# Optimization experiments

Measured on AMD Instinct MI355X. Metric: run time of the kernel, lower is better.

## Reference

```python
import jax, jax.numpy as jnp
import numpy as np

L_ITERS = 8   # number of ReduNet layers
C = 10        # number of classes
D = 1024      # feature dimension
N = 4096      # number of samples (columns of Z)


def setup_inputs() -> dict:
    key = jax.random.key(0)
    k0, k1, k2, k3 = jax.random.split(key, 4)
    Z = jax.random.normal(k0, (D, N), dtype=jnp.float32)
    # column-normalized features, as the net maintains at every layer
    Z = Z / jnp.linalg.norm(Z, axis=0, keepdims=True)
    # Elist[l]: (D,D) expansion operator; Cslist[l]: (C,D,D) per-class compression operators
    Elist = jax.random.normal(k1, (L_ITERS, D, D), dtype=jnp.float32) / np.float32(np.sqrt(D))
    Cslist = jax.random.normal(k2, (L_ITERS, C, D, D), dtype=jnp.float32) / np.float32(np.sqrt(D))
    gamma = jax.random.uniform(k3, (C,), dtype=jnp.float32)
    gamma = gamma / jnp.sum(gamma)
    eta = jnp.asarray(0.5, dtype=jnp.float32)
    temperature = jnp.asarray(0.1, dtype=jnp.float32)
    return {"Z": Z, "Elist": Elist, "Cslist": Cslist, "gamma": gamma,
            "eta": eta, "temperature": temperature, "L": L_ITERS}


def reference(Z, Elist, Cslist, gamma, eta, temperature, L):
    for l in range(L):
        Cs = Cslist[l]                                   # (C, d, d)
        CZ = jnp.einsum('cij,jn->cin', Cs, Z)            # (C, d, n)
        sims = -jnp.sqrt(jnp.sum(CZ * CZ, axis=1))       # fro norm over dim=1 -> (C, n)
        P_hat = jax.nn.softmax(sims / temperature, axis=0)  # softmax over classes
        PZ = P_hat[:, None, :] * Z                       # (C, d, n)
        term = jnp.einsum('c,cij,cjn->in', gamma, Cs, PZ)   # gamma-weighted class compression
        grads = Elist[l] @ Z - term                      # (d, n)
        Z = Z + eta * grads
        Z = Z / jnp.linalg.norm(Z, axis=0, keepdims=True)   # column-wise normalization
    return Z
```

## Files before the change

kernel.cpp:

```cpp
#include <hip/hip_runtime.h>
#include <hip/hip_bf16.h>
#include <stdint.h>

#define D_DIM 1024
#define N_DIM 4096
#define C_CLS 10
#define L_IT 8
#define M_DIM 11264
#define NBM 44

typedef __bf16 bf16_t;
typedef __bf16 bf16x8 __attribute__((ext_vector_type(8)));
typedef __bf16 bf16x4 __attribute__((ext_vector_type(4)));
typedef float  f32x4  __attribute__((ext_vector_type(4)));
typedef unsigned short u16x8 __attribute__((ext_vector_type(8)));

__device__ __forceinline__ float bf2f(uint16_t u) {
  union { uint32_t i; float f; } x; x.i = ((uint32_t)u) << 16; return x.f;
}

__global__ __launch_bounds__(256) void pack_w(const float4* __restrict__ Cs,
                                              const float4* __restrict__ El,
                                              bf16x4* __restrict__ dst) {
  const int CS4 = C_CLS * D_DIM * D_DIM / 4;
  int i = blockIdx.x * 256 + threadIdx.x;
  float4 v = (i < CS4) ? Cs[i] : El[i - CS4];
  bf16x4 o;
  o[0] = (bf16_t)v.x; o[1] = (bf16_t)v.y; o[2] = (bf16_t)v.z; o[3] = (bf16_t)v.w;
  dst[i] = o;
}

__global__ __launch_bounds__(256) void init_zt(const float* __restrict__ Zin,
                                               float* __restrict__ ZfT,
                                               bf16_t* __restrict__ ZbT) {
  __shared__ float tile[32][33];
  int tx = threadIdx.x & 31, ty = threadIdx.x >> 5;
  int nb = blockIdx.x, db = blockIdx.y;
  int n = nb * 32 + tx;
#pragma unroll
  for (int j = 0; j < 32; j += 8) {
    int d = db * 32 + ty + j;
    tile[ty + j][tx] = Zin[(size_t)d * N_DIM + n];
  }
  __syncthreads();
  int d2 = db * 32 + tx;
#pragma unroll
  for (int j = 0; j < 32; j += 8) {
    int n2 = nb * 32 + ty + j;
    float v = tile[tx][ty + j];
    ZfT[(size_t)n2 * D_DIM + d2] = v;
    ZbT[(size_t)n2 * D_DIM + d2] = (bf16_t)v;
  }
}

__global__ __launch_bounds__(256) void final_out(const float* __restrict__ ZfT,
                                                 float* __restrict__ outp) {
  __shared__ float tile[32][33];
  int tx = threadIdx.x & 31, ty = threadIdx.x >> 5;
  int nb = blockIdx.x, db = blockIdx.y;
#pragma unroll
  for (int j = 0; j < 32; j += 8) {
    int n = nb * 32 + ty + j;
    int d = db * 32 + tx;
    tile[ty + j][tx] = ZfT[(size_t)n * D_DIM + d];
  }
  __syncthreads();
#pragma unroll
  for (int j = 0; j < 32; j += 8) {
    int d2 = db * 32 + ty + j;
    int n2 = nb * 32 + tx;
    outp[(size_t)d2 * N_DIM + n2] = tile[tx][ty + j];
  }
}


#define STAGE_A(buf, h, t) do {                                                         \
    _Pragma("unroll") for (int e_ = 0; e_ < 2; ++e_) {                                  \
      const bf16_t* s_ = Wb + aoff0[e_] + (size_t)(h) * 65536 + (size_t)(t) * 64;       \
      __builtin_amdgcn_global_load_lds(                                                 \
        (const __attribute__((address_space(1))) void*)s_,                              \
        (__attribute__((address_space(3))) void*)(lds + (buf)*16384 + (h)*8192 + dstslot[e_]), \
        16, 0, 0);                                                                      \
    } } while (0)

#define STAGE_B(buf, h, t) do {                                                         \
    _Pragma("unroll") for (int e_ = 0; e_ < 2; ++e_) {                                  \
      const bf16_t* s_ = ZbT + boff0[e_] + (size_t)(h) * 32768 + (size_t)(t) * 64;      \
      __builtin_amdgcn_global_load_lds(                                                 \
        (const __attribute__((address_space(1))) void*)s_,                              \
        (__attribute__((address_space(3))) void*)(lds + 32768 + (buf)*16384 + (h)*8192 + dstslot[e_]), \
        16, 0, 0);                                                                      \
    } } while (0)

#define LOAD_A(buf, qm) do {                                                            \
    _Pragma("unroll") for (int f_ = 0; f_ < 4; ++f_)                                    \
      _Pragma("unroll") for (int kk_ = 0; kk_ < 2; ++kk_)                               \
        a[f_][kk_] = *(const bf16x8*)(lds + (buf)*16384 + (qm)*8192 + aRowBase + f_*1024 + sidx[kk_]); \
  } while (0)

#define LOAD_Bq(buf, qn, arr) do {                                                      \
    _Pragma("unroll") for (int f_ = 0; f_ < 2; ++f_)                                    \
      _Pragma("unroll") for (int kk_ = 0; kk_ < 2; ++kk_)                               \
        arr[f_][kk_] = *(const bf16x8*)(lds + 32768 + (buf)*16384 + (qn)*8192 + bRowBase + f_*1024 + sidx[kk_]); \
  } while (0)

#define MFMA_Q(qm, qn, arr) do {                                                        \
    _Pragma("unroll") for (int mm_ = 0; mm_ < 4; ++mm_)                                 \
      _Pragma("unroll") for (int nn_ = 0; nn_ < 2; ++nn_)                               \
        _Pragma("unroll") for (int kk_ = 0; kk_ < 2; ++kk_)                             \
          acc[(qm)*4+mm_][(qn)*2+nn_] = __builtin_amdgcn_mfma_f32_16x16x32_bf16(        \
            a[mm_][kk_], arr[nn_][kk_], acc[(qm)*4+mm_][(qn)*2+nn_], 0, 0, 0);          \
  } while (0)

#define PHASE(qm, qn, arr, LOAD_STMT, STAGE_STMT, WAIT_STMT) do {                       \
    LOAD_STMT;                                                                          \
    STAGE_STMT;                                                                         \
    __builtin_amdgcn_s_barrier();                                                       \
    asm volatile("s_waitcnt lgkmcnt(0)" ::: "memory");                                  \
    __builtin_amdgcn_sched_barrier(0);                                                  \
    __builtin_amdgcn_s_setprio(1);                                                      \
    MFMA_Q(qm, qn, arr);                                                                \
    __builtin_amdgcn_s_setprio(0);                                                      \
    WAIT_STMT;                                                                          \
    __builtin_amdgcn_s_barrier();                                                       \
  } while (0)

__global__ __launch_bounds__(512, 2) void gemm_wz8(const bf16_t* __restrict__ Wb,
                                                   const bf16_t* __restrict__ ZbT,
                                                   bf16_t* __restrict__ OUT_T, int ldn,
                                                   float* __restrict__ ssq) {
  __shared__ __align__(16) bf16_t lds[65536];

  int nwg = gridDim.x;
  int bid = blockIdx.x;
  int q = nwg >> 3, r = nwg & 7;
  int xcd = bid & 7, idx = bid >> 3;
  int swz = (xcd < r ? xcd * (q + 1) : r * (q + 1) + (xcd - r) * q) + idx;
  int bm = swz % NBM, bn = swz / NBM;
  int m0 = bm * 256, n0 = bn * 256;

  int tid = threadIdx.x;
  int wave = tid >> 6, lane = tid & 63;
  int wrow = wave >> 2, wcol = wave & 3;
  int lm = lane & 15, lks = lane >> 4;
  int sw = lm & 7;

  size_t aoff0[2], boff0[2];
  int dstslot[2];
#pragma unroll
  for (int e = 0; e < 2; ++e) {
    int j = e * 512 + tid;
    int rih = j >> 3, sl = j & 7;
    int sg = sl ^ (rih & 7);
    int arow = (rih & 63) + ((rih >> 6) << 7);
    int brow = (rih & 31) + ((rih >> 5) << 6);
    aoff0[e] = (size_t)(m0 + arow) * 1024 + sg * 8;
    boff0[e] = (size_t)(n0 + brow) * 1024 + sg * 8;
    dstslot[e] = e * 4096 + wave * 512;
  }

  int aRowBase = (wrow * 64 + lm) * 64;
  int bRowBase = (wcol * 32 + lm) * 64;
  int sidx[2] = { ((0 + lks) ^ sw) * 8, ((4 + lks) ^ sw) * 8 };

  f32x4 acc[8][4] = {};
  bf16x8 a[4][2], b0[2][2], b1[2][2];

  STAGE_A(0, 0, 0); STAGE_A(0, 1, 0); STAGE_B(0, 0, 0); STAGE_B(0, 1, 0);
  STAGE_A(1, 0, 1); STAGE_B(1, 0, 1);
  asm volatile("s_waitcnt vmcnt(4)" ::: "memory");
  __builtin_amdgcn_s_barrier();

  for (int it = 0; it < 7; ++it) {
    int tO = 2 * it + 1, tN = 2 * it + 2, tM = 2 * it + 3;
    PHASE(0, 0, b0, LOAD_A(0,0); LOAD_Bq(0,0,b0), STAGE_A(1, 1, tO), );
    PHASE(0, 1, b1, LOAD_Bq(0,1,b1),              STAGE_B(1, 1, tO), );
    PHASE(1, 0, b0, LOAD_A(0,1),                  STAGE_A(0, 0, tN), );
    PHASE(1, 1, b1, ,                             STAGE_A(0, 1, tN), asm volatile("s_waitcnt vmcnt(4)" ::: "memory"));
    PHASE(0, 0, b0, LOAD_A(1,0); LOAD_Bq(1,0,b0), STAGE_B(0, 0, tN), );
    PHASE(0, 1, b1, LOAD_Bq(1,1,b1),              STAGE_B(0, 1, tN), );
    PHASE(1, 0, b0, LOAD_A(1,1),                  STAGE_A(1, 0, tM), );
    PHASE(1, 1, b1, ,                             STAGE_B(1, 0, tM), asm volatile("s_waitcnt vmcnt(4)" ::: "memory"));
  }
  PHASE(0, 0, b0, LOAD_A(0,0); LOAD_Bq(0,0,b0), STAGE_A(1, 1, 15), );
  PHASE(0, 1, b1, LOAD_Bq(0,1,b1),              STAGE_B(1, 1, 15), );
  PHASE(1, 0, b0, LOAD_A(0,1),                  , );
  PHASE(1, 1, b1, ,                             , asm volatile("s_waitcnt vmcnt(0)" ::: "memory"));
  PHASE(0, 0, b0, LOAD_A(1,0); LOAD_Bq(1,0,b0), , );
  PHASE(0, 1, b1, LOAD_Bq(1,1,b1),              , );
  PHASE(1, 0, b0, LOAD_A(1,1),                  , );
  PHASE(1, 1, b1, ,                             , );

#pragma unroll
  for (int mf = 0; mf < 8; ++mf)
#pragma unroll
    for (int nf = 0; nf < 4; ++nf) {
      int col = n0 + wcol * 64 + nf * 16 + lm;
      int row = m0 + wrow * 128 + mf * 16 + lks * 4;
      bf16x4 v;
#pragma unroll
      for (int rr = 0; rr < 4; ++rr) v[rr] = (bf16_t)acc[mf][nf][rr];
      *(bf16x4*)(OUT_T + (size_t)col * M_DIM + row) = v;
    }

  if (m0 < C_CLS * 1024) {
    int c = m0 >> 10;
#pragma unroll
    for (int nf = 0; nf < 4; ++nf) {
      float v = 0.f;
#pragma unroll
      for (int mf = 0; mf < 8; ++mf)
#pragma unroll
        for (int rr = 0; rr < 4; ++rr)
          v += acc[mf][nf][rr] * acc[mf][nf][rr];
      v += __shfl_xor(v, 16);
      v += __shfl_xor(v, 32);
      if (lks == 0)
        atomicAdd(&ssq[(size_t)c * ldn + n0 + wcol * 64 + nf * 16 + lm], v);
    }
  }
}

__global__ __launch_bounds__(256) void update2(const bf16_t* __restrict__ OUT_T, int Nc,
                                               const float* __restrict__ ssq,
                                               const float* __restrict__ gamma,
                                               const float* __restrict__ etap,
                                               const float* __restrict__ tempr,
                                               float* __restrict__ ZfT,
                                               bf16_t* __restrict__ ZbT,
                                               int n_off) {
  int wv = threadIdx.x >> 6, lane = threadIdx.x & 63;
  int nl = blockIdx.x * 4 + wv;
  if (nl >= Nc) return;
  int n = n_off + nl;
  float eta = etap[0], invT = 1.0f / tempr[0];

  float s[C_CLS], m = -1e30f;
#pragma unroll
  for (int c = 0; c < C_CLS; ++c) {
    float sim = -sqrtf(ssq[(size_t)c * Nc + nl]);
    s[c] = sim;
    m = fmaxf(m, sim);
  }
  float sum = 0.f;
#pragma unroll
  for (int c = 0; c < C_CLS; ++c) {
    float e = __expf((s[c] - m) * invT);
    s[c] = e;
    sum += e;
  }
  float invsum = 1.0f / sum;
  float gP[C_CLS];
#pragma unroll
  for (int c = 0; c < C_CLS; ++c) gP[c] = gamma[c] * s[c] * invsum;

  const u16x8* ob = (const u16x8*)(OUT_T + (size_t)nl * M_DIM) + lane * 2;
  float term[16] = {};
#pragma unroll
  for (int c = 0; c < C_CLS; ++c) {
    u16x8 v0 = ob[c * 128], v1 = ob[c * 128 + 1];
#pragma unroll
    for (int j = 0; j < 8; ++j) {
      term[j]     += gP[c] * bf2f(v0[j]);
      term[8 + j] += gP[c] * bf2f(v1[j]);
    }
  }
  u16x8 g0 = ob[C_CLS * 128], g1 = ob[C_CLS * 128 + 1];

  const f32x4* zp = (const f32x4*)(ZfT + (size_t)n * D_DIM) + lane * 4;
  f32x4 z[4] = { zp[0], zp[1], zp[2], zp[3] };

  float zn[16];
  float ss = 0.f;
#pragma unroll
  for (int j = 0; j < 16; ++j) {
    float g = bf2f(j < 8 ? g0[j & 7] : g1[j & 7]);
    float v = z[j >> 2][j & 3] + eta * (g - term[j]);
    zn[j] = v;
    ss += v * v;
  }
#pragma unroll
  for (int k = 1; k < 64; k <<= 1) ss += __shfl_xor(ss, k);
  float inv = rsqrtf(ss);

  f32x4* zo = (f32x4*)(ZfT + (size_t)n * D_DIM) + lane * 4;
  bf16x8* bo = (bf16x8*)(ZbT + (size_t)n * D_DIM) + lane * 2;
#pragma unroll
  for (int q4 = 0; q4 < 4; ++q4) {
    f32x4 o;
#pragma unroll
    for (int j = 0; j < 4; ++j) o[j] = zn[q4 * 4 + j] * inv;
    zo[q4] = o;
  }
#pragma unroll
  for (int h = 0; h < 2; ++h) {
    bf16x8 o;
#pragma unroll
    for (int j = 0; j < 8; ++j) o[j] = (bf16_t)(zn[h * 8 + j] * inv);
    bo[h] = o;
  }
}

extern "C" void kernel_launch(void* const* d_in, const int* in_sizes, int n_in,
                              void* d_out, int out_size, void* d_ws, size_t ws_size,
                              hipStream_t stream) {
  (void)in_sizes; (void)n_in; (void)out_size;
  const float* Zin        = (const float*)d_in[0];
  const float* Elist      = (const float*)d_in[1];
  const float* Cslist     = (const float*)d_in[2];
  const float* gamma      = (const float*)d_in[3];
  const float* eta        = (const float*)d_in[4];
  const float* temperature= (const float*)d_in[5];

  auto align256 = [](size_t x) { return (x + 255) & ~(size_t)255; };
  size_t zbt_b = align256((size_t)N_DIM * D_DIM * 2);
  size_t zft_b = align256((size_t)N_DIM * D_DIM * 4);
  size_t wb_b  = align256((size_t)M_DIM * D_DIM * 2);
  size_t ssq_b = align256((size_t)L_IT * C_CLS * N_DIM * 4);
  size_t out_b = align256((size_t)M_DIM * N_DIM * 2);

  if (zbt_b + zft_b + wb_b + ssq_b + out_b > ws_size) {
    hipMemsetAsync(d_out, 0, (size_t)D_DIM * N_DIM * 4, stream);
    return;
  }

  char* p = (char*)d_ws;
  bf16_t* ZbT  = (bf16_t*)p; p += zbt_b;
  float*  ZfT  = (float*)p;  p += zft_b;
  bf16_t* Wb   = (bf16_t*)p; p += wb_b;
  float*  ssq  = (float*)p;  p += ssq_b;
  bf16_t* OUT_T= (bf16_t*)p;

  hipMemsetAsync(ssq, 0, (size_t)L_IT * C_CLS * N_DIM * 4, stream);
  init_zt<<<dim3(N_DIM / 32, D_DIM / 32), 256, 0, stream>>>(Zin, ZfT, ZbT);

  for (int l = 0; l < L_IT; ++l) {
    const float* Cs = Cslist + (size_t)l * C_CLS * D_DIM * D_DIM;
    const float* El = Elist  + (size_t)l * D_DIM * D_DIM;
    float* ssq_l = ssq + (size_t)l * C_CLS * N_DIM;

    pack_w<<<dim3(M_DIM * D_DIM / 4 / 256), 256, 0, stream>>>(
        (const float4*)Cs, (const float4*)El, (bf16x4*)Wb);

    gemm_wz8<<<dim3(NBM * (N_DIM / 256)), 512, 0, stream>>>(
        Wb, ZbT, OUT_T, N_DIM, ssq_l);
    update2<<<dim3(N_DIM / 4), 256, 0, stream>>>(
        OUT_T, N_DIM, ssq_l, gamma, eta, temperature, ZfT, ZbT, 0);
  }
  final_out<<<dim3(N_DIM / 32, D_DIM / 32), 256, 0, stream>>>(ZfT, (float*)d_out);
}
```

Measured before the change: 1.244 ms.

## Make the GEMM persistent over 256 workgroups and prefetch the next tile across tiles

Replaces the 704-workgroup GEMM launch with a persistent kernel of 256 workgroups. Each workgroup processes 2-3 output tiles inside its XCD-grouped range and stages the next tile's first K-slices during the tail of the current one, so the pipeline prologue and epilogue are overlapped. The phase schedule is also reworked to issue both B quarter loads together, with a partial lgkmcnt wait between the two MFMA quarters. This aims to remove the wave-quantization tail and per-tile pipeline fill cost. In exchange it adds a full vmcnt drain and accumulator reset between tiles, and some workgroups get 3 tiles while others get 2.

```diff
diff --git a/kernel.cpp b/kernel.cpp
--- a/kernel.cpp
+++ b/kernel.cpp
@@ -74,18 +74,18 @@
 }
 
 
-#define STAGE_A(buf, h, t) do {                                                         \
+#define SA(buf, h, ab, t) do {                                                          \
     _Pragma("unroll") for (int e_ = 0; e_ < 2; ++e_) {                                  \
-      const bf16_t* s_ = Wb + aoff0[e_] + (size_t)(h) * 65536 + (size_t)(t) * 64;       \
+      const bf16_t* s_ = Wb + (ab) + laneA[e_] + (size_t)(h) * 65536 + (size_t)(t) * 64;\
       __builtin_amdgcn_global_load_lds(                                                 \
         (const __attribute__((address_space(1))) void*)s_,                              \
         (__attribute__((address_space(3))) void*)(lds + (buf)*16384 + (h)*8192 + dstslot[e_]), \
         16, 0, 0);                                                                      \
     } } while (0)
 
-#define STAGE_B(buf, h, t) do {                                                         \
+#define SB(buf, h, bb, t) do {                                                          \
     _Pragma("unroll") for (int e_ = 0; e_ < 2; ++e_) {                                  \
-      const bf16_t* s_ = ZbT + boff0[e_] + (size_t)(h) * 32768 + (size_t)(t) * 64;      \
+      const bf16_t* s_ = ZbT + (bb) + laneB[e_] + (size_t)(h) * 32768 + (size_t)(t) * 64;\
       __builtin_amdgcn_global_load_lds(                                                 \
         (const __attribute__((address_space(1))) void*)s_,                              \
         (__attribute__((address_space(3))) void*)(lds + 32768 + (buf)*16384 + (h)*8192 + dstslot[e_]), \
@@ -104,7 +104,7 @@
         arr[f_][kk_] = *(const bf16x8*)(lds + 32768 + (buf)*16384 + (qn)*8192 + bRowBase + f_*1024 + sidx[kk_]); \
   } while (0)
 
-#define MFMA_Q(qm, qn, arr) do {                                                        \
+#define MFMAQ(qm, qn, arr) do {                                                         \
     _Pragma("unroll") for (int mm_ = 0; mm_ < 4; ++mm_)                                 \
       _Pragma("unroll") for (int nn_ = 0; nn_ < 2; ++nn_)                               \
         _Pragma("unroll") for (int kk_ = 0; kk_ < 2; ++kk_)                             \
@@ -112,32 +112,35 @@
             a[mm_][kk_], arr[nn_][kk_], acc[(qm)*4+mm_][(qn)*2+nn_], 0, 0, 0);          \
   } while (0)
 
-#define PHASE(qm, qn, arr, LOAD_STMT, STAGE_STMT, WAIT_STMT) do {                       \
-    LOAD_STMT;                                                                          \
-    STAGE_STMT;                                                                         \
-    __builtin_amdgcn_s_barrier();                                                       \
-    asm volatile("s_waitcnt lgkmcnt(0)" ::: "memory");                                  \
-    __builtin_amdgcn_sched_barrier(0);                                                  \
-    __builtin_amdgcn_s_setprio(1);                                                      \
-    MFMA_Q(qm, qn, arr);                                                                \
-    __builtin_amdgcn_s_setprio(0);                                                      \
-    WAIT_STMT;                                                                          \
-    __builtin_amdgcn_s_barrier();                                                       \
-  } while (0)
-
-__global__ __launch_bounds__(512, 2) void gemm_wz8(const bf16_t* __restrict__ Wb,
-                                                   const bf16_t* __restrict__ ZbT,
-                                                   bf16_t* __restrict__ OUT_T, int ldn,
-                                                   float* __restrict__ ssq) {
+#define BAR   __builtin_amdgcn_s_barrier()
+#define SB0   __builtin_amdgcn_sched_barrier(0)
+#define LGKM0 do { asm volatile("s_waitcnt lgkmcnt(0)" ::: "memory"); SB0; } while (0)
+#define LGKM8 do { asm volatile("s_waitcnt lgkmcnt(8)" ::: "memory"); SB0; } while (0)
+#define VM(n) asm volatile("s_waitcnt vmcnt(" #n ")" ::: "memory")
+#define PRIO1 __builtin_amdgcn_s_setprio(1)
+#define PRIO0 __builtin_amdgcn_s_setprio(0)
+
+__global__ __launch_bounds__(512, 2) void gemm_persist(const bf16_t* __restrict__ Wb,
+                                                       const bf16_t* __restrict__ ZbT,
+                                                       bf16_t* __restrict__ OUT_T,
+                                                       float* __restrict__ ssq) {
   __shared__ __align__(16) bf16_t lds[65536];
 
-  int nwg = gridDim.x;
   int bid = blockIdx.x;
-  int q = nwg >> 3, r = nwg & 7;
-  int xcd = bid & 7, idx = bid >> 3;
-  int swz = (xcd < r ? xcd * (q + 1) : r * (q + 1) + (xcd - r) * q) + idx;
-  int bm = swz % NBM, bn = swz / NBM;
-  int m0 = bm * 256, n0 = bn * 256;
+  int x = bid & 7, kb = bid >> 3;
+  int nt, b88;
+  if (kb < 24) { b88 = 3 * kb; nt = 3; }
+  else         { b88 = 72 + 2 * (kb - 24); nt = 2; }
+  int m0s[3], n0s[3];
+  size_t tA[3], tB[3];
+#pragma unroll
+  for (int i = 0; i < 3; ++i) {
+    int g = x * 88 + b88 + (i < nt ? i : nt - 1);
+    m0s[i] = (g % NBM) * 256;
+    n0s[i] = (g / NBM) * 256;
+    tA[i] = (size_t)m0s[i] * 1024;
+    tB[i] = (size_t)n0s[i] * 1024;
+  }
 
   int tid = threadIdx.x;
   int wave = tid >> 6, lane = tid & 63;
@@ -145,7 +148,7 @@
   int lm = lane & 15, lks = lane >> 4;
   int sw = lm & 7;
 
-  size_t aoff0[2], boff0[2];
+  size_t laneA[2], laneB[2];
   int dstslot[2];
 #pragma unroll
   for (int e = 0; e < 2; ++e) {
@@ -154,8 +157,8 @@
     int sg = sl ^ (rih & 7);
     int arow = (rih & 63) + ((rih >> 6) << 7);
     int brow = (rih & 31) + ((rih >> 5) << 6);
-    aoff0[e] = (size_t)(m0 + arow) * 1024 + sg * 8;
-    boff0[e] = (size_t)(n0 + brow) * 1024 + sg * 8;
+    laneA[e] = (size_t)arow * 1024 + sg * 8;
+    laneB[e] = (size_t)brow * 1024 + sg * 8;
     dstslot[e] = e * 4096 + wave * 512;
   }
 
@@ -166,58 +169,78 @@
   f32x4 acc[8][4] = {};
   bf16x8 a[4][2], b0[2][2], b1[2][2];
 
-  STAGE_A(0, 0, 0); STAGE_A(0, 1, 0); STAGE_B(0, 0, 0); STAGE_B(0, 1, 0);
-  STAGE_A(1, 0, 1); STAGE_B(1, 0, 1);
-  asm volatile("s_waitcnt vmcnt(4)" ::: "memory");
-  __builtin_amdgcn_s_barrier();
-
-  for (int it = 0; it < 7; ++it) {
-    int tO = 2 * it + 1, tN = 2 * it + 2, tM = 2 * it + 3;
-    PHASE(0, 0, b0, LOAD_A(0,0); LOAD_Bq(0,0,b0), STAGE_A(1, 1, tO), );
-    PHASE(0, 1, b1, LOAD_Bq(0,1,b1),              STAGE_B(1, 1, tO), );
-    PHASE(1, 0, b0, LOAD_A(0,1),                  STAGE_A(0, 0, tN), );
-    PHASE(1, 1, b1, ,                             STAGE_A(0, 1, tN), asm volatile("s_waitcnt vmcnt(4)" ::: "memory"));
-    PHASE(0, 0, b0, LOAD_A(1,0); LOAD_Bq(1,0,b0), STAGE_B(0, 0, tN), );
-    PHASE(0, 1, b1, LOAD_Bq(1,1,b1),              STAGE_B(0, 1, tN), );
-    PHASE(1, 0, b0, LOAD_A(1,1),                  STAGE_A(1, 0, tM), );
-    PHASE(1, 1, b1, ,                             STAGE_B(1, 0, tM), asm volatile("s_waitcnt vmcnt(4)" ::: "memory"));
-  }
-  PHASE(0, 0, b0, LOAD_A(0,0); LOAD_Bq(0,0,b0), STAGE_A(1, 1, 15), );
-  PHASE(0, 1, b1, LOAD_Bq(0,1,b1),              STAGE_B(1, 1, 15), );
-  PHASE(1, 0, b0, LOAD_A(0,1),                  , );
-  PHASE(1, 1, b1, ,                             , asm volatile("s_waitcnt vmcnt(0)" ::: "memory"));
-  PHASE(0, 0, b0, LOAD_A(1,0); LOAD_Bq(1,0,b0), , );
-  PHASE(0, 1, b1, LOAD_Bq(1,1,b1),              , );
-  PHASE(1, 0, b0, LOAD_A(1,1),                  , );
-  PHASE(1, 1, b1, ,                             , );
-
-#pragma unroll
-  for (int mf = 0; mf < 8; ++mf)
-#pragma unroll
-    for (int nf = 0; nf < 4; ++nf) {
-      int col = n0 + wcol * 64 + nf * 16 + lm;
-      int row = m0 + wrow * 128 + mf * 16 + lks * 4;
-      bf16x4 v;
-#pragma unroll
-      for (int rr = 0; rr < 4; ++rr) v[rr] = (bf16_t)acc[mf][nf][rr];
-      *(bf16x4*)(OUT_T + (size_t)col * M_DIM + row) = v;
+  SA(0, 0, tA[0], 0); SA(0, 1, tA[0], 0); SB(0, 0, tB[0], 0); SB(0, 1, tB[0], 0);
+  SA(1, 0, tA[0], 1); SB(1, 0, tB[0], 1);
+  VM(4);
+  BAR;
+
+  for (int tt = 0; tt < nt; ++tt) {
+    size_t aC = tA[tt], bC = tB[tt];
+    int nx = (tt + 1 < nt) ? tt + 1 : tt;
+    bool hn = (tt + 1 < nt);
+    size_t aN = tA[nx], bN = tB[nx];
+
+    for (int it = 0; it < 8; ++it) {
+      int tO = 2 * it + 1, tn2 = 2 * it + 2, tm2 = 2 * it + 3;
+      bool l7 = (it == 7);
+
+      LOAD_A(0, 0); LOAD_Bq(0, 0, b0); LOAD_Bq(0, 1, b1);
+      SA(1, 1, aC, tO); SB(1, 1, bC, tO);
+      BAR; LGKM8; PRIO1; MFMAQ(0, 0, b0); LGKM0; MFMAQ(0, 1, b1); PRIO0; BAR;
+
+      LOAD_A(0, 1);
+      if (!l7)      SA(0, 0, aC, tn2);
+      else if (hn)  SA(0, 0, aN, 0);
+      BAR; LGKM0; PRIO1; MFMAQ(1, 0, b0); MFMAQ(1, 1, b1); PRIO0;
+      if (l7 && !hn) { VM(0); } else { VM(2); }
+      BAR;
+
+      LOAD_A(1, 0); LOAD_Bq(1, 0, b0); LOAD_Bq(1, 1, b1);
+      if (!l7)      { SA(0, 1, aC, tn2); SB(0, 0, bC, tn2); SB(0, 1, bC, tn2); }
+      else if (hn)  { SA(0, 1, aN, 0);   SB(0, 0, bN, 0);   SB(0, 1, bN, 0);   }
+      BAR; LGKM8; PRIO1; MFMAQ(0, 0, b0); LGKM0; MFMAQ(0, 1, b1); PRIO0; BAR;
+
+      LOAD_A(1, 1);
+      if (!l7)      { SA(1, 0, aC, tm2); SB(1, 0, bC, tm2); }
+      else if (hn)  { SA(1, 0, aN, 1);   SB(1, 0, bN, 1);   }
+      BAR; LGKM0; PRIO1; MFMAQ(1, 0, b0); MFMAQ(1, 1, b1); PRIO0;
+      VM(4);
+      BAR;
     }
 
-  if (m0 < C_CLS * 1024) {
-    int c = m0 >> 10;
-#pragma unroll
-    for (int nf = 0; nf < 4; ++nf) {
-      float v = 0.f;
-#pragma unroll
-      for (int mf = 0; mf < 8; ++mf)
-#pragma unroll
-        for (int rr = 0; rr < 4; ++rr)
-          v += acc[mf][nf][rr] * acc[mf][nf][rr];
-      v += __shfl_xor(v, 16);
-      v += __shfl_xor(v, 32);
-      if (lks == 0)
-        atomicAdd(&ssq[(size_t)c * ldn + n0 + wcol * 64 + nf * 16 + lm], v);
+    int m0 = m0s[tt], n0 = n0s[tt];
+#pragma unroll
+    for (int mf = 0; mf < 8; ++mf)
+#pragma unroll
+      for (int nf = 0; nf < 4; ++nf) {
+        int col = n0 + wcol * 64 + nf * 16 + lm;
+        int row = m0 + wrow * 128 + mf * 16 + lks * 4;
+        bf16x4 v;
+#pragma unroll
+        for (int rr = 0; rr < 4; ++rr) v[rr] = (bf16_t)acc[mf][nf][rr];
+        *(bf16x4*)(OUT_T + (size_t)col * M_DIM + row) = v;
+      }
+    if (m0 < C_CLS * 1024) {
+      int c = m0 >> 10;
+#pragma unroll
+      for (int nf = 0; nf < 4; ++nf) {
+        float v = 0.f;
+#pragma unroll
+        for (int mf = 0; mf < 8; ++mf)
+#pragma unroll
+          for (int rr = 0; rr < 4; ++rr)
+            v += acc[mf][nf][rr] * acc[mf][nf][rr];
+        v += __shfl_xor(v, 16);
+        v += __shfl_xor(v, 32);
+        if (lks == 0)
+          atomicAdd(&ssq[(size_t)c * N_DIM + n0 + wcol * 64 + nf * 16 + lm], v);
+      }
     }
+    asm volatile("s_waitcnt vmcnt(0)" ::: "memory");
+#pragma unroll
+    for (int mf = 0; mf < 8; ++mf)
+#pragma unroll
+      for (int nf = 0; nf < 4; ++nf) acc[mf][nf] = (f32x4)(0.f);
   }
 }
 
@@ -342,8 +365,7 @@
     pack_w<<<dim3(M_DIM * D_DIM / 4 / 256), 256, 0, stream>>>(
         (const float4*)Cs, (const float4*)El, (bf16x4*)Wb);
 
-    gemm_wz8<<<dim3(NBM * (N_DIM / 256)), 512, 0, stream>>>(
-        Wb, ZbT, OUT_T, N_DIM, ssq_l);
+    gemm_persist<<<dim3(256), 512, 0, stream>>>(Wb, ZbT, OUT_T, ssq_l);
     update2<<<dim3(N_DIM / 4), 256, 0, stream>>>(
         OUT_T, N_DIM, ssq_l, gamma, eta, temperature, ZfT, ZbT, 0);
   }
```

After: 1.281 ms. 1.03x slower.

## Restructure GEMM main loop into four phases per K-step with merged B loads

Applied to the files above, without the earlier changes.

Rewrites the software pipeline of the bf16 MFMA GEMM so that each phase loads both B quarter-fragments and issues MFMAs for a full M-half, halving the number of barrier pairs per K-tile from eight to four. Global-to-LDS staging is regrouped so all B halves for a tile are issued together, and waits are relaxed to vmcnt(8). The explicit lgkmcnt(0) wait and sched_barrier before MFMAs are dropped, and the epilogue is folded into the loop with a conditional stage flag. Fewer barriers should cut synchronization stalls, but holding more B fragments live raises register pressure, and removing the explicit LDS wait relies on compiler-inserted waits.

```diff
diff --git a/kernel.cpp b/kernel.cpp
--- a/kernel.cpp
+++ b/kernel.cpp
@@ -74,7 +74,7 @@
 }
 
 
-#define STAGE_A(buf, h, t) do {                                                         \
+#define SA(buf, h, t) do {                                                              \
     _Pragma("unroll") for (int e_ = 0; e_ < 2; ++e_) {                                  \
       const bf16_t* s_ = Wb + aoff0[e_] + (size_t)(h) * 65536 + (size_t)(t) * 64;       \
       __builtin_amdgcn_global_load_lds(                                                 \
@@ -83,7 +83,7 @@
         16, 0, 0);                                                                      \
     } } while (0)
 
-#define STAGE_B(buf, h, t) do {                                                         \
+#define SBst(buf, h, t) do {                                                            \
     _Pragma("unroll") for (int e_ = 0; e_ < 2; ++e_) {                                  \
       const bf16_t* s_ = ZbT + boff0[e_] + (size_t)(h) * 32768 + (size_t)(t) * 64;      \
       __builtin_amdgcn_global_load_lds(                                                 \
@@ -104,7 +104,7 @@
         arr[f_][kk_] = *(const bf16x8*)(lds + 32768 + (buf)*16384 + (qn)*8192 + bRowBase + f_*1024 + sidx[kk_]); \
   } while (0)
 
-#define MFMA_Q(qm, qn, arr) do {                                                        \
+#define MFMAQ(qm, qn, arr) do {                                                         \
     _Pragma("unroll") for (int mm_ = 0; mm_ < 4; ++mm_)                                 \
       _Pragma("unroll") for (int nn_ = 0; nn_ < 2; ++nn_)                               \
         _Pragma("unroll") for (int kk_ = 0; kk_ < 2; ++kk_)                             \
@@ -112,17 +112,21 @@
             a[mm_][kk_], arr[nn_][kk_], acc[(qm)*4+mm_][(qn)*2+nn_], 0, 0, 0);          \
   } while (0)
 
-#define PHASE(qm, qn, arr, LOAD_STMT, STAGE_STMT, WAIT_STMT) do {                       \
-    LOAD_STMT;                                                                          \
-    STAGE_STMT;                                                                         \
-    __builtin_amdgcn_s_barrier();                                                       \
-    asm volatile("s_waitcnt lgkmcnt(0)" ::: "memory");                                  \
-    __builtin_amdgcn_sched_barrier(0);                                                  \
-    __builtin_amdgcn_s_setprio(1);                                                      \
-    MFMA_Q(qm, qn, arr);                                                                \
-    __builtin_amdgcn_s_setprio(0);                                                      \
-    WAIT_STMT;                                                                          \
-    __builtin_amdgcn_s_barrier();                                                       \
+#define BAR   __builtin_amdgcn_s_barrier()
+#define VM(n) asm volatile("s_waitcnt vmcnt(" #n ")" ::: "memory")
+#define PRIO1 __builtin_amdgcn_s_setprio(1)
+#define PRIO0 __builtin_amdgcn_s_setprio(0)
+
+#define PH(qm, LOADS, STAGES, WAIT) do {                                                \
+    LOADS;                                                                              \
+    STAGES;                                                                             \
+    BAR;                                                                                \
+    PRIO1;                                                                              \
+    MFMAQ(qm, 0, b0);                                                                   \
+    MFMAQ(qm, 1, b1);                                                                   \
+    PRIO0;                                                                              \
+    WAIT;                                                                               \
+    BAR;                                                                                \
   } while (0)
 
 __global__ __launch_bounds__(512, 2) void gemm_wz8(const bf16_t* __restrict__ Wb,
@@ -166,30 +170,39 @@
   f32x4 acc[8][4] = {};
   bf16x8 a[4][2], b0[2][2], b1[2][2];
 
-  STAGE_A(0, 0, 0); STAGE_A(0, 1, 0); STAGE_B(0, 0, 0); STAGE_B(0, 1, 0);
-  STAGE_A(1, 0, 1); STAGE_B(1, 0, 1);
-  asm volatile("s_waitcnt vmcnt(4)" ::: "memory");
-  __builtin_amdgcn_s_barrier();
-
-  for (int it = 0; it < 7; ++it) {
+  SA(0, 0, 0); SBst(0, 0, 0); SBst(0, 1, 0);
+  SA(0, 1, 0);
+  SA(1, 0, 1); SBst(1, 0, 1); SBst(1, 1, 1);
+  VM(8);
+  BAR;
+
+  for (int it = 0; it < 8; ++it) {
     int tO = 2 * it + 1, tN = 2 * it + 2, tM = 2 * it + 3;
-    PHASE(0, 0, b0, LOAD_A(0,0); LOAD_Bq(0,0,b0), STAGE_A(1, 1, tO), );
-    PHASE(0, 1, b1, LOAD_Bq(0,1,b1),              STAGE_B(1, 1, tO), );
-    PHASE(1, 0, b0, LOAD_A(0,1),                  STAGE_A(0, 0, tN), );
-    PHASE(1, 1, b1, ,                             STAGE_A(0, 1, tN), asm volatile("s_waitcnt vmcnt(4)" ::: "memory"));
-    PHASE(0, 0, b0, LOAD_A(1,0); LOAD_Bq(1,0,b0), STAGE_B(0, 0, tN), );
-    PHASE(0, 1, b1, LOAD_Bq(1,1,b1),              STAGE_B(0, 1, tN), );
-    PHASE(1, 0, b0, LOAD_A(1,1),                  STAGE_A(1, 0, tM), );
-    PHASE(1, 1, b1, ,                             STAGE_B(1, 0, tM), asm volatile("s_waitcnt vmcnt(4)" ::: "memory"));
-  }
-  PHASE(0, 0, b0, LOAD_A(0,0); LOAD_Bq(0,0,b0), STAGE_A(1, 1, 15), );
-  PHASE(0, 1, b1, LOAD_Bq(0,1,b1),              STAGE_B(1, 1, 15), );
-  PHASE(1, 0, b0, LOAD_A(0,1),                  , );
-  PHASE(1, 1, b1, ,                             , asm volatile("s_waitcnt vmcnt(0)" ::: "memory"));
-  PHASE(0, 0, b0, LOAD_A(1,0); LOAD_Bq(1,0,b0), , );
-  PHASE(0, 1, b1, LOAD_Bq(1,1,b1),              , );
-  PHASE(1, 0, b0, LOAD_A(1,1),                  , );
-  PHASE(1, 1, b1, ,                             , );
+    bool st = (it < 7);
+
+    PH(0,
+       LOAD_A(0, 0); LOAD_Bq(0, 0, b0); LOAD_Bq(0, 1, b1),
+       SA(1, 1, tO),
+       VM(8));
+
+    if (st) {
+      PH(1, LOAD_A(0, 1), SA(0, 0, tN); SBst(0, 0, tN); SBst(0, 1, tN), VM(8));
+    } else {
+      PH(1, LOAD_A(0, 1), , VM(2));
+    }
+
+    if (st) {
+      PH(0, LOAD_A(1, 0); LOAD_Bq(1, 0, b0); LOAD_Bq(1, 1, b1), SA(0, 1, tN), VM(8));
+    } else {
+      PH(0, LOAD_A(1, 0); LOAD_Bq(1, 0, b0); LOAD_Bq(1, 1, b1), , VM(0));
+    }
+
+    if (st) {
+      PH(1, LOAD_A(1, 1), SA(1, 0, tM); SBst(1, 0, tM); SBst(1, 1, tM), VM(8));
+    } else {
+      PH(1, LOAD_A(1, 1), , );
+    }
+  }
 
 #pragma unroll
   for (int mf = 0; mf < 8; ++mf)
```

Result: no change. 1.258 ms (+1.1%).
